# Kernel tuning notes

Hardware: AMD Instinct MI355X
Metric: run time of the kernel (lower is better)

## Reference

```python
import jax, jax.numpy as jnp
import numpy as np

NEG_FILL = -9e15  # matches torch masked_fill value

def setup_inputs() -> dict:
    key = jax.random.key(0)
    k1, k2, k3 = jax.random.split(key, 3)
    shape = (1, 16, 4096, 64)  # [batch, heads, seq, d_head]
    q = jax.random.normal(k1, shape, dtype=jnp.float32)
    k = jax.random.normal(k2, shape, dtype=jnp.float32)
    v = jax.random.normal(k3, shape, dtype=jnp.float32)
    return {"q": q, "k": k, "v": v}

def reference(q, k, v):
    d_k = q.shape[-1]
    S_q, S_k = q.shape[-2], k.shape[-2]
    # scores: [b, h, s_q, s_k]
    scores = jnp.einsum('bhqd,bhkd->bhqk', q, k) / jnp.sqrt(jnp.float32(d_k))
    # causal mask (lower triangular allowed)
    causal = jnp.tril(jnp.ones((S_q, S_k), dtype=bool))
    scores = jnp.where(causal, scores, jnp.float32(NEG_FILL))
    attn = jax.nn.softmax(scores, axis=-1)
    return jnp.einsum('bhqk,bhkd->bhqd', attn, v)
```

## Files before the change

kernel.cpp:

```cpp
#include <hip/hip_runtime.h>

#define SS 4096
#define DD 64
#define NH 16
#define QB 128
#define NQB (SS / QB)
#define KVT 64
#define NKV (SS / KVT)
#define TILE_BYTES 8192

typedef float  fx4    __attribute__((ext_vector_type(4)));
typedef __bf16 bf16x8 __attribute__((ext_vector_type(8)));
typedef short  sx4    __attribute__((ext_vector_type(4)));

typedef __attribute__((address_space(1))) const unsigned int GU32;
typedef __attribute__((address_space(3))) unsigned int       LU32;

__device__ __forceinline__ void gload16(const void* g, void* l) {
    __builtin_amdgcn_global_load_lds((GU32*)g, (LU32*)l, 16, 0, 0);
}

__device__ __forceinline__ float fast_exp2(float x) {
    return __builtin_amdgcn_exp2f(x);
}

__global__ __launch_bounds__(256)
void prep_kernel(const float* __restrict__ Kg, const float* __restrict__ Vg,
                 char* __restrict__ Kimg, char* __restrict__ Vimg)
{
    __shared__ __bf16 lv[64][72];
    const int tid = threadIdx.x;
    const int h = (int)blockIdx.x >> 6;
    const int t = (int)blockIdx.x & 63;
    const int r = tid >> 2;
    const size_t rowbase = ((size_t)h * SS + (size_t)t * KVT) * DD;

    {
        char* kdst = Kimg + (size_t)(h * NKV + t) * TILE_BYTES;
        const float* src = Kg + rowbase + (size_t)r * DD;
#pragma unroll
        for (int cc = 0; cc < 2; ++cc) {
            const int c = (tid & 3) * 2 + cc;
            fx4 f0 = *(const fx4*)(src + c * 8);
            fx4 f1 = *(const fx4*)(src + c * 8 + 4);
            bf16x8 b;
#pragma unroll
            for (int j = 0; j < 4; ++j) { b[j] = (__bf16)f0[j]; b[4 + j] = (__bf16)f1[j]; }
            *(bf16x8*)(kdst + r * 128 + ((c ^ (r & 7)) << 4)) = b;
        }
    }

    {
        const float* src = Vg + rowbase + (size_t)r * DD + (tid & 3) * 16;
#pragma unroll
        for (int qq = 0; qq < 4; ++qq) {
            fx4 f = *(const fx4*)(src + qq * 4);
#pragma unroll
            for (int j = 0; j < 4; ++j) lv[r][(tid & 3) * 16 + qq * 4 + j] = (__bf16)f[j];
        }
    }
    __syncthreads();
    {
        char* vdst = Vimg + (size_t)(h * NKV + t) * TILE_BYTES;
        const int d = r;
#pragma unroll
        for (int cc = 0; cc < 2; ++cc) {
            const int c = (tid & 3) * 2 + cc;
            bf16x8 b;
#pragma unroll
            for (int j = 0; j < 8; ++j) b[j] = lv[c * 8 + j][d];
            *(bf16x8*)(vdst + d * 128 + ((c ^ (d & 7)) << 4)) = b;
        }
    }
}

__global__ __launch_bounds__(256, 4)
void attn_fwd(const float* __restrict__ Qg, const char* __restrict__ Kimg,
              const char* __restrict__ Vimg, float* __restrict__ Og,
              unsigned short* __restrict__ accY, float* __restrict__ lmW)
{
    __shared__ __align__(16) char lK[2][TILE_BYTES];
    __shared__ __align__(16) char lV[2][TILE_BYTES];

    const int tid  = threadIdx.x;
    const int wid  = tid >> 6;
    const int lane = tid & 63;
    const int lr   = lane & 15;
    const int g    = lane >> 4;

    const int b  = (int)blockIdx.x;
    const int h  = b & 15;
    const int j  = b >> 4;
    const int hi = j >> 5;
    const int ii = j & 31;
    const int c  = (ii >> 4) & 1;
    const int kk4 = ii & 15;
    const int p  = hi ? (15 - kk4) : (16 + kk4);

    const int t0 = c ? (p + 1) : 0;
    const int t1 = c ? (2 * p + 2) : (p + 1);

    const int q0 = p * QB + wid * 32;

    const float* Qh = Qg + (size_t)h * SS * DD;
    float*       Oh = Og + (size_t)h * SS * DD;
    const char*  Kh = Kimg + (size_t)(h * NKV) * TILE_BYTES;
    const char*  Vh = Vimg + (size_t)(h * NKV) * TILE_BYTES;

    const float QSCALE = 0.125f * 1.44269504088896f;

    bf16x8 qa[2][2];
#pragma unroll
    for (int u = 0; u < 2; ++u) {
        const int qrow = q0 + 16 * u + lr;
#pragma unroll
        for (int h2 = 0; h2 < 2; ++h2) {
            const float* src = Qh + (size_t)qrow * DD + h2 * 32 + g * 8;
            fx4 f0 = *(const fx4*)(src);
            fx4 f1 = *(const fx4*)(src + 4);
            bf16x8 tq;
#pragma unroll
            for (int jj = 0; jj < 4; ++jj) {
                tq[jj]     = (__bf16)(f0[jj] * QSCALE);
                tq[jj + 4] = (__bf16)(f1[jj] * QSCALE);
            }
            qa[u][h2] = tq;
        }
    }

    fx4 acc[2][4];
#pragma unroll
    for (int u = 0; u < 2; ++u)
#pragma unroll
        for (int d0 = 0; d0 < 4; ++d0) acc[u][d0] = (fx4){0.f, 0.f, 0.f, 0.f};
    float m_run = -1e30f;
    float l_run[2] = {0.f, 0.f};

#define STAGE(buf, tt)                                                          \
    do {                                                                        \
        const char* img_ = (wid < 2) ? Kh : Vh;                                 \
        char* dst_ = ((wid < 2) ? &lK[buf][0] : &lV[buf][0]) + (wid & 1) * 4096;\
        const char* src_ = img_ + (size_t)(tt) * TILE_BYTES + (wid & 1) * 4096  \
                           + lane * 16;                                         \
        gload16(src_,        dst_);                                             \
        gload16(src_ + 1024, dst_ + 1024);                                      \
        gload16(src_ + 2048, dst_ + 2048);                                      \
        gload16(src_ + 3072, dst_ + 3072);                                      \
    } while (0)

    STAGE(0, t0);
    __syncthreads();

    int cur = 0;
    for (int t = t0; t < t1; ++t) {
        if (t + 1 < t1) STAGE(cur ^ 1, t + 1);

        float s[2][4][4];
        __builtin_amdgcn_s_setprio(1);
#pragma unroll
        for (int ks = 0; ks < 4; ++ks) {
            const int row = ks * 16 + lr;
            const char* base = &lK[cur][row * 128];
            const bf16x8 ka0 = *(const bf16x8*)(base + (((g    ) ^ (row & 7)) << 4));
            const bf16x8 ka1 = *(const bf16x8*)(base + (((g ^ 4) ^ (row & 7)) << 4));
#pragma unroll
            for (int u = 0; u < 2; ++u) {
                fx4 st = (fx4){0.f, 0.f, 0.f, 0.f};
                st = __builtin_amdgcn_mfma_f32_16x16x32_bf16(ka0, qa[u][0], st, 0, 0, 0);
                st = __builtin_amdgcn_mfma_f32_16x16x32_bf16(ka1, qa[u][1], st, 0, 0, 0);
#pragma unroll
                for (int r = 0; r < 4; ++r) s[u][ks][r] = st[r];
            }
        }
        __builtin_amdgcn_s_setprio(0);

        if (t >= 2 * p) {
            const int kv0 = t * KVT;
#pragma unroll
            for (int u = 0; u < 2; ++u) {
                const int qrow = q0 + 16 * u + lr;
#pragma unroll
                for (int ks = 0; ks < 4; ++ks)
#pragma unroll
                    for (int r = 0; r < 4; ++r) {
                        const int kvi = kv0 + ks * 16 + 4 * g + r;
                        if (kvi > qrow) s[u][ks][r] = -1e30f;
                    }
            }
        }

        float m4[2][4];
#pragma unroll
        for (int u = 0; u < 2; ++u)
#pragma unroll
            for (int ks = 0; ks < 4; ++ks)
                m4[u][ks] = fmaxf(fmaxf(s[u][ks][0], s[u][ks][1]),
                                  fmaxf(s[u][ks][2], s[u][ks][3]));
        const float tm = fmaxf(
            fmaxf(fmaxf(m4[0][0], m4[0][1]), fmaxf(m4[0][2], m4[0][3])),
            fmaxf(fmaxf(m4[1][0], m4[1][1]), fmaxf(m4[1][2], m4[1][3])));

        if (__any(tm > m_run + 8.0f)) {
            float wm = tm;
            wm = fmaxf(wm, __shfl_xor(wm, 1));
            wm = fmaxf(wm, __shfl_xor(wm, 2));
            wm = fmaxf(wm, __shfl_xor(wm, 4));
            wm = fmaxf(wm, __shfl_xor(wm, 8));
            wm = fmaxf(wm, __shfl_xor(wm, 16));
            wm = fmaxf(wm, __shfl_xor(wm, 32));
            const float alpha = fast_exp2(m_run - wm);
            m_run = wm;
            l_run[0] *= alpha; l_run[1] *= alpha;
#pragma unroll
            for (int u = 0; u < 2; ++u)
#pragma unroll
                for (int d0 = 0; d0 < 4; ++d0) {
                    fx4 a = acc[u][d0];
                    a[0] *= alpha; a[1] *= alpha; a[2] *= alpha; a[3] *= alpha;
                    acc[u][d0] = a;
                }
        }

        sx4 pa[2][4];
#pragma unroll
        for (int u = 0; u < 2; ++u) {
            float e[4][4];
#pragma unroll
            for (int ks = 0; ks < 4; ++ks)
#pragma unroll
                for (int r = 0; r < 4; ++r)
                    e[ks][r] = fast_exp2(s[u][ks][r] - m_run);
            const float u0 = (e[0][0] + e[0][1]) + (e[0][2] + e[0][3]);
            const float u1 = (e[1][0] + e[1][1]) + (e[1][2] + e[1][3]);
            const float u2 = (e[2][0] + e[2][1]) + (e[2][2] + e[2][3]);
            const float u3 = (e[3][0] + e[3][1]) + (e[3][2] + e[3][3]);
            l_run[u] += (u0 + u1) + (u2 + u3);
#pragma unroll
            for (int ks = 0; ks < 4; ++ks) {
                sx4 t4;
#pragma unroll
                for (int jj = 0; jj < 4; ++jj) {
                    const __bf16 pb = (__bf16)e[ks][jj];
                    t4[jj] = __builtin_bit_cast(short, pb);
                }
                pa[u][ks] = t4;
            }
        }

        __builtin_amdgcn_s_setprio(1);
#pragma unroll
        for (int ks = 0; ks < 4; ++ks) {
            const int s0 = ks * 2 + (g >> 1);
#pragma unroll
            for (int d0 = 0; d0 < 4; ++d0) {
                const int row = d0 * 16 + lr;
                const sx4 vb = *(const sx4*)(&lV[cur][row * 128 +
                                ((s0 ^ (row & 7)) << 4) + (g & 1) * 8]);
                acc[0][d0] = __builtin_amdgcn_mfma_f32_16x16x16bf16_1k(pa[0][ks], vb, acc[0][d0], 0, 0, 0);
                acc[1][d0] = __builtin_amdgcn_mfma_f32_16x16x16bf16_1k(pa[1][ks], vb, acc[1][d0], 0, 0, 0);
            }
        }
        __builtin_amdgcn_s_setprio(0);

        if (t + 1 < t1) __syncthreads();
        cur ^= 1;
    }

    float ls0 = l_run[0];
    ls0 += __shfl_xor(ls0, 16);
    ls0 += __shfl_xor(ls0, 32);
    float ls1 = l_run[1];
    ls1 += __shfl_xor(ls1, 16);
    ls1 += __shfl_xor(ls1, 32);

    const int lmb = (h * 32 + p) * 128 + wid * 32 + lr;

    if (c == 0) {
#pragma unroll
        for (int u = 0; u < 2; ++u)
#pragma unroll
            for (int d0 = 0; d0 < 4; ++d0)
#pragma unroll
                for (int r = 0; r < 4; ++r)
                    Oh[(size_t)(q0 + 16 * u + 4 * g + r) * DD + d0 * 16 + lr] = acc[u][d0][r];
        if (lane < 16) {
            lmW[lmb]               = m_run;
            lmW[lmb + 16]          = m_run;
            lmW[65536 + lmb]       = ls0;
            lmW[65536 + lmb + 16]  = ls1;
        }
    } else {
        const size_t ab = (size_t)((h * 32 + p) * 128 + wid * 32) * 64;
#pragma unroll
        for (int u = 0; u < 2; ++u)
#pragma unroll
            for (int d0 = 0; d0 < 4; ++d0)
#pragma unroll
                for (int r = 0; r < 4; ++r) {
                    const __bf16 pb = (__bf16)acc[u][d0][r];
                    accY[ab + (size_t)(16 * u + 4 * g + r) * 64 + d0 * 16 + lr] =
                        __builtin_bit_cast(unsigned short, pb);
                }
        if (lane < 16) {
            lmW[131072 + lmb]      = m_run;
            lmW[131072 + lmb + 16] = m_run;
            lmW[196608 + lmb]      = ls0;
            lmW[196608 + lmb + 16] = ls1;
        }
    }
#undef STAGE
}

__global__ __launch_bounds__(256)
void combine_kernel(float* __restrict__ Og, const unsigned short* __restrict__ accY,
                    const float* __restrict__ lmW)
{
    const int blk = (int)blockIdx.x;
    const int h = blk >> 5, p = blk & 31;
    const int t = threadIdx.x;
    const int col = t & 63;
    const int r0  = t >> 6;
    const int lmbase = (h * 32 + p) * 128;
    const size_t obase = ((size_t)h * SS + (size_t)p * QB) * DD;
    const size_t ybase = (size_t)lmbase * 64;

    for (int rr = 0; rr < 32; ++rr) {
        const int row = rr * 4 + r0;
        const float m0 = lmW[lmbase + row];
        const float l0 = lmW[65536 + lmbase + row];
        const float m1 = lmW[131072 + lmbase + row];
        const float l1 = lmW[196608 + lmbase + row];
        const float mm = fmaxf(m0, m1);
        const float a  = fast_exp2(m0 - mm);
        const float bb = fast_exp2(m1 - mm);
        const float den = a * l0 + bb * l1;
        const size_t oi = obase + (size_t)row * DD + col;
        const unsigned int yb = ((unsigned int)accY[ybase + (size_t)row * 64 + col]) << 16;
        const float yv = __builtin_bit_cast(float, yb);
        Og[oi] = (a * Og[oi] + bb * yv) / den;
    }
}

extern "C" void kernel_launch(void* const* d_in, const int* in_sizes, int n_in,
                              void* d_out, int out_size, void* d_ws, size_t ws_size,
                              hipStream_t stream)
{
    (void)in_sizes; (void)n_in; (void)out_size; (void)ws_size;
    const float* q = (const float*)d_in[0];
    const float* k = (const float*)d_in[1];
    const float* v = (const float*)d_in[2];
    float*       o = (float*)d_out;

    char* ws = (char*)d_ws;
    char*           Kimg = ws;
    char*           Vimg = ws + ((size_t)1 << 23);
    unsigned short* accY = (unsigned short*)(ws + ((size_t)2 << 23));
    float*          lmW  = (float*)(ws + ((size_t)3 << 23));

    hipLaunchKernelGGL(prep_kernel,    dim3(NH * NKV), dim3(256), 0, stream, k, v, Kimg, Vimg);
    hipLaunchKernelGGL(attn_fwd,       dim3(1024),     dim3(256), 0, stream, q, Kimg, Vimg, o, accY, lmW);
    hipLaunchKernelGGL(combine_kernel, dim3(512),      dim3(256), 0, stream, o, accY, lmW);
}
```

Baseline: 85.40 us.

## Split causal KV range into variable chunk counts per query block

Replaces the fixed split of each query block into two KV halves with a variable number of chunks that grows with the query block's position. Each head gets 144 work items, so every block covers a roughly equal number of KV tiles. The combine kernel now merges n partial results using per-chunk max and sum statistics. This aims to balance load across the grid and cut tail imbalance. In exchange it writes more bf16 partial accumulators to the workspace and adds serial merge work in the combine step.

New measurement: 211.9 us. 2.48x slower.

```diff
diff --git a/kernel.cpp b/kernel.cpp
--- a/kernel.cpp
+++ b/kernel.cpp
@@ -8,6 +8,9 @@
 #define KVT 64
 #define NKV (SS / KVT)
 #define TILE_BYTES 8192
+
+#define CHUNKS_PER_H 144
+#define ACCW_PER_H   112
 
 typedef float  fx4    __attribute__((ext_vector_type(4)));
 typedef __bf16 bf16x8 __attribute__((ext_vector_type(8)));
@@ -77,7 +80,7 @@
 __global__ __launch_bounds__(256, 4)
 void attn_fwd(const float* __restrict__ Qg, const char* __restrict__ Kimg,
               const char* __restrict__ Vimg, float* __restrict__ Og,
-              unsigned short* __restrict__ accY, float* __restrict__ lmW)
+              unsigned short* __restrict__ accW, float* __restrict__ lmW)
 {
     __shared__ __align__(16) char lK[2][TILE_BYTES];
     __shared__ __align__(16) char lV[2][TILE_BYTES];
@@ -88,17 +91,26 @@
     const int lr   = lane & 15;
     const int g    = lane >> 4;
 
-    const int b  = (int)blockIdx.x;
-    const int h  = b & 15;
-    const int j  = b >> 4;
-    const int hi = j >> 5;
-    const int ii = j & 31;
-    const int c  = (ii >> 4) & 1;
-    const int kk4 = ii & 15;
-    const int p  = hi ? (15 - kk4) : (16 + kk4);
-
-    const int t0 = c ? (p + 1) : 0;
-    const int t1 = c ? (2 * p + 2) : (p + 1);
+    const int b = (int)blockIdx.x;
+    const int h = b / CHUNKS_PER_H;
+    int r_ = (CHUNKS_PER_H - 1) - (b - h * CHUNKS_PER_H);
+    const int cid = r_;
+    int m = 0;
+#pragma unroll
+    for (int i = 0; i < 7; ++i) {
+        if (r_ >= 4 * (i + 1)) { r_ -= 4 * (i + 1); m = i + 1; }
+    }
+    int p4 = 0;
+#pragma unroll
+    for (int i = 0; i < 3; ++i) {
+        if (r_ >= m + 1) { r_ -= (m + 1); ++p4; }
+    }
+    const int p  = 4 * m + p4;
+    const int ci = r_;
+    const int n  = m + 1;
+    const int W  = 2 * p + 2;
+    const int t0 = (ci * W) / n;
+    const int t1 = ((ci + 1) * W) / n;
 
     const int q0 = p * QB + wid * 32;
 
@@ -273,9 +285,15 @@
     ls1 += __shfl_xor(ls1, 16);
     ls1 += __shfl_xor(ls1, 32);
 
-    const int lmb = (h * 32 + p) * 128 + wid * 32 + lr;
-
-    if (c == 0) {
+    const int rowb = (h * CHUNKS_PER_H + cid) * 128 + wid * 32 + lr;
+    if (lane < 16) {
+        lmW[rowb]                = m_run;
+        lmW[rowb + 16]           = m_run;
+        lmW[294912 + rowb]       = ls0;
+        lmW[294912 + rowb + 16]  = ls1;
+    }
+
+    if (ci == 0) {
 #pragma unroll
         for (int u = 0; u < 2; ++u)
 #pragma unroll
@@ -283,14 +301,9 @@
 #pragma unroll
                 for (int r = 0; r < 4; ++r)
                     Oh[(size_t)(q0 + 16 * u + 4 * g + r) * DD + d0 * 16 + lr] = acc[u][d0][r];
-        if (lane < 16) {
-            lmW[lmb]               = m_run;
-            lmW[lmb + 16]          = m_run;
-            lmW[65536 + lmb]       = ls0;
-            lmW[65536 + lmb + 16]  = ls1;
-        }
     } else {
-        const size_t ab = (size_t)((h * 32 + p) * 128 + wid * 32) * 64;
+        const size_t ab = ((size_t)(h * ACCW_PER_H) + (cid - p - 1)) * 8192
+                        + (size_t)(wid * 32) * 64;
 #pragma unroll
         for (int u = 0; u < 2; ++u)
 #pragma unroll
@@ -298,46 +311,45 @@
 #pragma unroll
                 for (int r = 0; r < 4; ++r) {
                     const __bf16 pb = (__bf16)acc[u][d0][r];
-                    accY[ab + (size_t)(16 * u + 4 * g + r) * 64 + d0 * 16 + lr] =
+                    accW[ab + (size_t)(16 * u + 4 * g + r) * 64 + d0 * 16 + lr] =
                         __builtin_bit_cast(unsigned short, pb);
                 }
-        if (lane < 16) {
-            lmW[131072 + lmb]      = m_run;
-            lmW[131072 + lmb + 16] = m_run;
-            lmW[196608 + lmb]      = ls0;
-            lmW[196608 + lmb + 16] = ls1;
-        }
     }
 #undef STAGE
 }
 
 __global__ __launch_bounds__(256)
-void combine_kernel(float* __restrict__ Og, const unsigned short* __restrict__ accY,
+void combine_kernel(float* __restrict__ Og, const unsigned short* __restrict__ accW,
                     const float* __restrict__ lmW)
 {
     const int blk = (int)blockIdx.x;
     const int h = blk >> 5, p = blk & 31;
-    const int t = threadIdx.x;
-    const int col = t & 63;
-    const int r0  = t >> 6;
-    const int lmbase = (h * 32 + p) * 128;
+    const int m = p >> 2, n = m + 1;
+    const int cid0 = 2 * m * (m + 1) + (p & 3) * n;
+    const int lmB  = (h * CHUNKS_PER_H + cid0) * 128;
     const size_t obase = ((size_t)h * SS + (size_t)p * QB) * DD;
-    const size_t ybase = (size_t)lmbase * 64;
+    const size_t ab0   = ((size_t)(h * ACCW_PER_H) + (cid0 - p)) * 8192;
+
+    const int col = threadIdx.x & 63;
+    const int r0  = threadIdx.x >> 6;
 
     for (int rr = 0; rr < 32; ++rr) {
         const int row = rr * 4 + r0;
-        const float m0 = lmW[lmbase + row];
-        const float l0 = lmW[65536 + lmbase + row];
-        const float m1 = lmW[131072 + lmbase + row];
-        const float l1 = lmW[196608 + lmbase + row];
-        const float mm = fmaxf(m0, m1);
-        const float a  = fast_exp2(m0 - mm);
-        const float bb = fast_exp2(m1 - mm);
-        const float den = a * l0 + bb * l1;
+        float mm = lmW[lmB + row];
+        for (int i = 1; i < n; ++i) mm = fmaxf(mm, lmW[lmB + i * 128 + row]);
+
+        const float w0  = fast_exp2(lmW[lmB + row] - mm);
+        float den = w0 * lmW[294912 + lmB + row];
         const size_t oi = obase + (size_t)row * DD + col;
-        const unsigned int yb = ((unsigned int)accY[ybase + (size_t)row * 64 + col]) << 16;
-        const float yv = __builtin_bit_cast(float, yb);
-        Og[oi] = (a * Og[oi] + bb * yv) / den;
+        float val = w0 * Og[oi];
+        for (int i = 1; i < n; ++i) {
+            const float wi = fast_exp2(lmW[lmB + i * 128 + row] - mm);
+            den += wi * lmW[294912 + lmB + i * 128 + row];
+            const unsigned int ub =
+                ((unsigned int)accW[ab0 + (size_t)(i - 1) * 8192 + row * 64 + col]) << 16;
+            val += wi * __builtin_bit_cast(float, ub);
+        }
+        Og[oi] = val / den;
     }
 }
 
@@ -354,10 +366,10 @@
     char* ws = (char*)d_ws;
     char*           Kimg = ws;
     char*           Vimg = ws + ((size_t)1 << 23);
-    unsigned short* accY = (unsigned short*)(ws + ((size_t)2 << 23));
-    float*          lmW  = (float*)(ws + ((size_t)3 << 23));
-
-    hipLaunchKernelGGL(prep_kernel,    dim3(NH * NKV), dim3(256), 0, stream, k, v, Kimg, Vimg);
-    hipLaunchKernelGGL(attn_fwd,       dim3(1024),     dim3(256), 0, stream, q, Kimg, Vimg, o, accY, lmW);
-    hipLaunchKernelGGL(combine_kernel, dim3(512),      dim3(256), 0, stream, o, accY, lmW);
-}
+    unsigned short* accW = (unsigned short*)(ws + ((size_t)2 << 23));
+    float*          lmW  = (float*)(ws + ((size_t)2 << 23) + 29360128);
+
+    hipLaunchKernelGGL(prep_kernel,    dim3(NH * NKV),        dim3(256), 0, stream, k, v, Kimg, Vimg);
+    hipLaunchKernelGGL(attn_fwd,       dim3(NH * CHUNKS_PER_H), dim3(256), 0, stream, q, Kimg, Vimg, o, accW, lmW);
+    hipLaunchKernelGGL(combine_kernel, dim3(512),             dim3(256), 0, stream, o, accW, lmW);
+}
```
